# Kernel tuning notes

Hardware: AMD Instinct MI355X
Metric: run time of the kernel (lower is better)

## Reference

```python
import jax, jax.numpy as jnp
import numpy as np

SIGNAL = (32, 32)
KERNEL = (8, 8)
N_FEATURES = [64, 128, 128]
BATCH = 64
ALPHA = 0.5          # source references an undefined global `alpha`; fixed here
LEAKY_SLOPE = 0.01   # torch F.leaky_relu default


def _join_tensor(S, K, loc):
    i = np.arange(S)[:, None, None]
    j = np.arange(S)[None, :, None]
    k = np.arange(K)[None, None, :]
    M = (j >= i) & (i == np.maximum(j, k + loc))
    return jnp.asarray(M.astype(np.float32))


def _meet_tensor(S, K, loc):
    i = np.arange(S)[:, None, None]
    j = np.arange(S)[None, :, None]
    k = np.arange(K)[None, None, :]
    M = (j >= i) & (i == np.minimum(j, k + loc))
    return jnp.asarray(M.astype(np.float32))


def setup_inputs() -> dict:
    key = jax.random.key(0)
    sx, sy = SIGNAL
    kx, ky = KERNEL
    # meet layers use kernel_loc = signal - kernel; join layers use (0, 0)
    cmx = _meet_tensor(sx, kx, sx - kx)
    cmy = _meet_tensor(sy, ky, sy - ky)
    cjx = _join_tensor(sx, kx, 0)
    cjy = _join_tensor(sy, ky, 0)

    keys = jax.random.split(key, 16)
    x = jax.random.normal(keys[0], (BATCH, N_FEATURES[0], sx, sy), dtype=jnp.float32)

    def kaiming(k, shape):
        fan_in = shape[0] * shape[1] * shape[2]  # kx*ky*in_features
        return jax.random.normal(k, shape, dtype=jnp.float32) * np.float32(np.sqrt(2.0 / fan_in))

    inp = {"x": x, "cmx": cmx, "cmy": cmy, "cjx": cjx, "cjy": cjy}
    for li in range(len(N_FEATURES) - 1):
        fi, fo = N_FEATURES[li], N_FEATURES[li + 1]
        inp[f"mw{li}"] = kaiming(keys[1 + 2 * li], (kx, ky, fi, fo))
        inp[f"mb{li}"] = jnp.zeros((fo, 1, 1), dtype=jnp.float32)
        inp[f"jw{li}"] = kaiming(keys[2 + 2 * li], (kx, ky, fi, fo))
        inp[f"jb{li}"] = jnp.zeros((fo, 1, 1), dtype=jnp.float32)
    return inp


def _lattice_conv(cx, cy, X, W, b):
    # Y[m,g,x,y] = sum_{i,j,a,b} cx[i,x,a] cy[j,y,b] X[m,f,i,j] W[a,b,f,g] + bias
    return jnp.einsum('ixa,jyb,mfij,abfg->mgxy', cx, cy, X, W, optimize='optimal') + b


def reference(x, cmx, cmy, cjx, cjy, mw0, mb0, jw0, jb0, mw1, mb1, jw1, jb1):
    params = [(mw0, mb0, jw0, jb0), (mw1, mb1, jw1, jb1)]
    for mw, mb, jw, jb in params:
        m = _lattice_conv(cmx, cmy, x, mw, mb)
        j = _lattice_conv(cjx, cjy, x, jw, jb)
        x = jax.nn.leaky_relu((1.0 - ALPHA) * m + ALPHA * j, negative_slope=LEAKY_SLOPE)
    return x
```

## Files before the change

kernel.cpp:

```cpp
#include <hip/hip_runtime.h>
#include <stdint.h>


typedef __attribute__((ext_vector_type(8))) short short8;
typedef __attribute__((ext_vector_type(4))) float floatx4;

__device__ __forceinline__ float bf2f(unsigned short u) {
  union { uint32_t u; float f; } c; c.u = ((uint32_t)u) << 16; return c.f;
}
__device__ __forceinline__ unsigned short f2bf(float f) {
  union { float f; uint32_t u; } c; c.f = f;
  uint32_t u = c.u;
  uint32_t r = (u + 0x7FFFu + ((u >> 16) & 1u)) >> 16;
  return (unsigned short)r;
}

__global__ void detect_dtype(const unsigned short* __restrict__ xa,
                             int* __restrict__ flag) {
  __shared__ int cnt;
  if (threadIdx.x == 0) cnt = 0;
  __syncthreads();
  unsigned short v = xa[threadIdx.x];
  int e = (v >> 7) & 0xFF;
  int ok = (v == 0) || (e >= 110 && e <= 140);
  atomicAdd(&cnt, ok);
  __syncthreads();
  if (threadIdx.x == 0) *flag = (cnt >= 240) ? 0 : 1;
}

__global__ __launch_bounds__(256) void transpose_in(
    const unsigned short* __restrict__ s16, const float* __restrict__ s32,
    unsigned short* __restrict__ dst, int R, int C,
    const int* __restrict__ flag) {
  __shared__ unsigned short tile[32][33];
  int fp32 = *flag;
  int tx = threadIdx.x, ty = threadIdx.y;
  int c0 = blockIdx.x * 32, r0 = blockIdx.y * 32;
  if (fp32) {
#pragma unroll
    for (int i = 0; i < 32; i += 8)
      tile[ty + i][tx] = f2bf(s32[(size_t)(r0 + ty + i) * C + (c0 + tx)]);
  } else {
#pragma unroll
    for (int i = 0; i < 32; i += 8)
      tile[ty + i][tx] = s16[(size_t)(r0 + ty + i) * C + (c0 + tx)];
  }
  __syncthreads();
#pragma unroll
  for (int i = 0; i < 32; i += 8)
    dst[(size_t)(c0 + ty + i) * R + (r0 + tx)] = tile[tx][ty + i];
}

__global__ __launch_bounds__(256) void transpose_out(
    const unsigned short* __restrict__ src, unsigned short* __restrict__ d16,
    float* __restrict__ d32, int R, int C, const int* __restrict__ flag) {
  __shared__ unsigned short tile[32][33];
  int fp32 = *flag;
  int tx = threadIdx.x, ty = threadIdx.y;
  int c0 = blockIdx.x * 32, r0 = blockIdx.y * 32;
#pragma unroll
  for (int i = 0; i < 32; i += 8)
    tile[ty + i][tx] = src[(size_t)(r0 + ty + i) * C + (c0 + tx)];
  __syncthreads();
  if (fp32) {
#pragma unroll
    for (int i = 0; i < 32; i += 8)
      d32[(size_t)(c0 + ty + i) * R + (r0 + tx)] = bf2f(tile[tx][ty + i]);
  } else {
#pragma unroll
    for (int i = 0; i < 32; i += 8)
      d16[(size_t)(c0 + ty + i) * R + (r0 + tx)] = tile[tx][ty + i];
  }
}

__global__ __launch_bounds__(256) void transpose_w(
    const void* __restrict__ mw, const void* __restrict__ jw,
    float* __restrict__ mwT, float* __restrict__ jwT, int C,
    const int* __restrict__ flag) {
  const void* src = blockIdx.z ? jw : mw;
  float* dst = blockIdx.z ? jwT : mwT;
  __shared__ float tile[32][33];
  int fp32 = *flag;
  int tx = threadIdx.x, ty = threadIdx.y;
  int c0 = blockIdx.x * 32, r0 = blockIdx.y * 32;
#pragma unroll
  for (int i = 0; i < 32; i += 8) {
    size_t idx = (size_t)(r0 + ty + i) * C + (c0 + tx);
    tile[ty + i][tx] = fp32 ? ((const float*)src)[idx]
                            : bf2f(((const unsigned short*)src)[idx]);
  }
  __syncthreads();
#pragma unroll
  for (int i = 0; i < 32; i += 8)
    dst[(size_t)(c0 + ty + i) * 64 + (r0 + tx)] = tile[tx][ty + i];
}

#define SLOT_W1 0
#define SLOT_SB 225
#define SLOT_AS 289
#define SLOT_M  353
#define N_SLOTS 417

template <int F, int G>
__global__ __launch_bounds__(256) void prep_weights2(
    const float* __restrict__ mwT, const float* __restrict__ jwT,
    unsigned short* __restrict__ Wall) {
  int tid = blockIdx.x * 256 + threadIdx.x;
  if (tid >= F * G) return;
  int group = blockIdx.y;
  int f = tid % F, g = tid / F;
  const size_t WS = (size_t)G * F;
  unsigned short* wout = Wall + (size_t)g * F + f;

  float w[64];
  {
    const float4* p = (const float4*)(mwT + (size_t)(f * G + g) * 64);
#pragma unroll
    for (int i = 0; i < 16; ++i) {
      float4 v = p[i];
      w[4 * i] = v.x; w[4 * i + 1] = v.y; w[4 * i + 2] = v.z; w[4 * i + 3] = v.w;
    }
  }
  if (group == 3) {
#pragma unroll
    for (int ab = 0; ab < 64; ++ab)
      wout[(size_t)(SLOT_M + ab) * WS] = f2bf(0.5f * w[ab]);
    return;
  }
#pragma unroll
  for (int a = 0; a < 8; ++a)
#pragma unroll
    for (int b = 6; b >= 0; --b) w[a * 8 + b] += w[a * 8 + b + 1];
  if (group == 2) {
#pragma unroll
    for (int ab = 0; ab < 64; ++ab)
      wout[(size_t)(SLOT_AS + ab) * WS] = f2bf(0.5f * w[ab]);
  }
#pragma unroll
  for (int a = 6; a >= 0; --a)
#pragma unroll
    for (int b = 0; b < 8; ++b) w[a * 8 + b] += w[(a + 1) * 8 + b];
  if (group == 2) {
#pragma unroll
    for (int px = 0; px < 8; ++px)
#pragma unroll
      for (int b = 0; b < 8; ++b) {
        float v = w[px * 8 + b] - (b < 7 ? w[px * 8 + b + 1] : 0.0f);
        wout[(size_t)(SLOT_SB + px * 8 + b) * WS] = f2bf(0.5f * v);
      }
    return;
  }
  float pp[64];
  {
    const float4* p = (const float4*)(jwT + (size_t)(f * G + g) * 64);
#pragma unroll
    for (int i = 0; i < 16; ++i) {
      float4 v = p[i];
      pp[4 * i] = v.x; pp[4 * i + 1] = v.y; pp[4 * i + 2] = v.z; pp[4 * i + 3] = v.w;
    }
  }
#pragma unroll
  for (int a = 0; a < 8; ++a)
#pragma unroll
    for (int b = 1; b < 8; ++b) pp[a * 8 + b] += pp[a * 8 + b - 1];
#pragma unroll
  for (int a = 1; a < 8; ++a)
#pragma unroll
    for (int b = 0; b < 8; ++b) pp[a * 8 + b] += pp[(a - 1) * 8 + b];
  int cx0 = (group == 0) ? 0 : 7, cx1 = (group == 0) ? 7 : 15;
  for (int cx = cx0; cx < cx1; ++cx) {
    int pmx = cx < 7 ? cx : 7;
    int pxx = cx > 7 ? cx - 7 : 0;
#pragma unroll
    for (int cy = 0; cy < 15; ++cy) {
      int pmy = cy < 7 ? cy : 7;
      int pyy = cy > 7 ? cy - 7 : 0;
      float v = 0.5f * (w[pxx * 8 + pyy] + pp[pmx * 8 + pmy]);
      wout[(size_t)(SLOT_W1 + cx * 15 + cy) * WS] = f2bf(v);
    }
  }
}

__global__ void prep_bias2(const void* __restrict__ mb0,
                           const void* __restrict__ jb0,
                           const void* __restrict__ mb1,
                           const void* __restrict__ jb1,
                           float* __restrict__ bias0,
                           float* __restrict__ bias1,
                           const int* __restrict__ flag) {
  int fp32 = *flag;
  int g = threadIdx.x & 127;
  const void* mb = (threadIdx.x < 128) ? mb0 : mb1;
  const void* jb = (threadIdx.x < 128) ? jb0 : jb1;
  float* bo = (threadIdx.x < 128) ? bias0 : bias1;
  float m = fp32 ? ((const float*)mb)[g] : bf2f(((const unsigned short*)mb)[g]);
  float j = fp32 ? ((const float*)jb)[g] : bf2f(((const unsigned short*)jb)[g]);
  bo[g] = 0.5f * (m + j);
}

template <int F>
__device__ __forceinline__ void mfma_tile(
    const unsigned short* __restrict__ A, const unsigned short* __restrict__ W,
    floatx4 acc[8], int wave, int n, int q) {
  const unsigned short* a_ptr = A + ((size_t)(wave * 16 + n)) * F + q * 8;
  const unsigned short* w_ptr = W + (size_t)n * F + q * 8;
#pragma unroll
  for (int kk = 0; kk < F; kk += 32) {
    short8 av = *(const short8*)(a_ptr + kk);
#pragma unroll
    for (int t = 0; t < 8; ++t) {
      short8 bv = *(const short8*)(w_ptr + (size_t)t * 16 * F + kk);
      acc[t] = __builtin_amdgcn_mfma_f32_16x16x32_bf16(av, bv, acc[t], 0, 0, 0);
    }
  }
}

template <int F>
__global__ __launch_bounds__(256) void corr_gemm(
    const unsigned short* __restrict__ Xt, const unsigned short* __restrict__ Wall,
    float* __restrict__ V, float* __restrict__ U, float* __restrict__ T) {
  int bid = blockIdx.x;
  int wave = threadIdx.x >> 6, lane = threadIdx.x & 63;
  int n = lane & 15, q = lane >> 4;
  int ipos, slot;
  float* out;
  if (bid < 256) {
    int a = bid >> 5, y = bid & 31;
    int py = y > 24 ? y - 24 : 0;
    ipos = (24 + a) * 32 + y;
    slot = SLOT_AS + a * 8 + py;
    out = V + (size_t)(a * 32 + y) * 8192;
  } else if (bid < 512) {
    int i = bid - 256;
    int b = i >> 5, x = i & 31;
    int px = x > 24 ? x - 24 : 0;
    ipos = x * 32 + 24 + b;
    slot = SLOT_SB + px * 8 + b;
    out = U + (size_t)(b * 32 + x) * 8192;
  } else {
    int i = bid - 512;
    int a = i >> 3, b = i & 7;
    ipos = (24 + a) * 32 + 24 + b;
    slot = SLOT_M + a * 8 + b;
    out = T + (size_t)(a * 8 + b) * 8192;
  }
  floatx4 acc[8];
#pragma unroll
  for (int t = 0; t < 8; ++t) acc[t] = (floatx4){0.f, 0.f, 0.f, 0.f};
  mfma_tile<F>(Xt + (size_t)ipos * 64 * F, Wall + (size_t)slot * 128 * F,
               acc, wave, n, q);
#pragma unroll
  for (int t = 0; t < 8; ++t) {
    int gcol = t * 16 + n;
#pragma unroll
    for (int r = 0; r < 4; ++r) {
      int m = wave * 16 + q * 4 + r;
      out[(size_t)m * 128 + gcol] = acc[t][r];
    }
  }
}

__global__ __launch_bounds__(256) void scan_corr(float* __restrict__ V,
                                                 float* __restrict__ U,
                                                 float* __restrict__ T) {
  int b = blockIdx.x;
  if (b < 2048) {
    float* base = (b < 1024) ? V : U;
    int tid = ((b & 1023) * 256 + threadIdx.x);
    float* p = base + (size_t)tid;
    float s = 0.f;
#pragma unroll
    for (int a = 0; a < 8; ++a) {
      s += p[(size_t)a * 262144];
      p[(size_t)a * 262144] = s;
    }
  } else {
    int mg = (b - 2048) * 256 + threadIdx.x;
    float col[8];
#pragma unroll
    for (int i = 0; i < 8; ++i) col[i] = 0.f;
#pragma unroll
    for (int a = 0; a < 8; ++a) {
      float rs = 0.f;
#pragma unroll
      for (int bb = 0; bb < 8; ++bb) {
        size_t idx = (size_t)(a * 8 + bb) * 8192 + mg;
        col[bb] += T[idx];
        rs += col[bb];
        T[idx] = rs;
      }
    }
  }
}

template <int F>
__global__ __launch_bounds__(256) void final_gemm(
    const unsigned short* __restrict__ Xt, const unsigned short* __restrict__ Wall,
    const float* __restrict__ V, const float* __restrict__ U,
    const float* __restrict__ T, const float* __restrict__ bias,
    unsigned short* __restrict__ Out) {
  int pos = blockIdx.x;
  int x = pos >> 5, y = pos & 31;
  int wave = threadIdx.x >> 6, lane = threadIdx.x & 63;
  int n = lane & 15, q = lane >> 4;
  int clsx = x < 7 ? x : (x <= 24 ? 7 : x - 17);
  int clsy = y < 7 ? y : (y <= 24 ? 7 : y - 17);
  int px = x > 24 ? x - 24 : 0;
  int py = y > 24 ? y - 24 : 0;
  floatx4 acc[8];
#pragma unroll
  for (int t = 0; t < 8; ++t) acc[t] = (floatx4){0.f, 0.f, 0.f, 0.f};
  mfma_tile<F>(Xt + (size_t)pos * 64 * F,
               Wall + (size_t)(SLOT_W1 + clsx * 15 + clsy) * 128 * F,
               acc, wave, n, q);
  const float* c3 = px ? V + ((size_t)(px - 1) * 32 + y) * 8192 : nullptr;
  const float* c2 = py ? U + ((size_t)(py - 1) * 32 + x) * 8192 : nullptr;
  const float* c4 =
      (px && py) ? T + (size_t)((px - 1) * 8 + (py - 1)) * 8192 : nullptr;
  unsigned short* o = Out + (size_t)pos * 64 * 128;
#pragma unroll
  for (int t = 0; t < 8; ++t) {
    int gcol = t * 16 + n;
    float bv = bias[gcol];
#pragma unroll
    for (int r = 0; r < 4; ++r) {
      int m = wave * 16 + q * 4 + r;
      size_t idx = (size_t)m * 128 + gcol;
      float v = acc[t][r] + bv;
      if (c3) v += c3[idx];
      if (c2) v += c2[idx];
      if (c4) v += c4[idx];
      v = v > 0.f ? v : 0.01f * v;
      o[idx] = f2bf(v);
    }
  }
}

extern "C" void kernel_launch(void* const* d_in, const int* in_sizes, int n_in,
                              void* d_out, int out_size, void* d_ws,
                              size_t ws_size, hipStream_t stream) {
  const void* x   = d_in[0];
  const void* mw0 = d_in[5];
  const void* mb0 = d_in[6];
  const void* jw0 = d_in[7];
  const void* jb0 = d_in[8];
  const void* mw1 = d_in[9];
  const void* mb1 = d_in[10];
  const void* jw1 = d_in[11];
  const void* jb1 = d_in[12];

  char* ws = (char*)d_ws;
  const size_t MB = 1u << 20;
  float*          mwT  = (float*)(ws + 0);
  float*          jwT  = (float*)(ws + 4 * MB + (512u << 10));
  unsigned short* Xt0  = (unsigned short*)(ws + 9 * MB);
  unsigned short* Out2 = (unsigned short*)(ws + 0);
  unsigned short* A1   = (unsigned short*)(ws + 18 * MB);
  unsigned short* WallR = (unsigned short*)(ws + 35 * MB);
  float* bias0 = (float*)(ws + 49 * MB);
  float* bias1 = bias0 + 128;
  int*   flag  = (int*)(bias1 + 128);
  float* V = (float*)d_out;
  float* U = V + (size_t)8 * 32 * 8192;
  float* T = U + (size_t)8 * 32 * 8192;

  detect_dtype<<<1, 256, 0, stream>>>((const unsigned short*)x, flag);

  dim3 tb(32, 8);
  transpose_in<<<dim3(32, 128), tb, 0, stream>>>(
      (const unsigned short*)x, (const float*)x, Xt0, 4096, 1024, flag);
  prep_bias2<<<1, 256, 0, stream>>>(mb0, jb0, mb1, jb1, bias0, bias1, flag);

  transpose_w<<<dim3(8192 / 32, 2, 2), tb, 0, stream>>>(mw0, jw0, mwT, jwT,
                                                        8192, flag);
  prep_weights2<64, 128><<<dim3(32, 4), 256, 0, stream>>>(mwT, jwT, WallR);
  corr_gemm<64><<<576, 256, 0, stream>>>(Xt0, WallR, V, U, T);
  scan_corr<<<2080, 256, 0, stream>>>(V, U, T);
  final_gemm<64><<<1024, 256, 0, stream>>>(Xt0, WallR, V, U, T, bias0, A1);

  transpose_w<<<dim3(16384 / 32, 2, 2), tb, 0, stream>>>(mw1, jw1, mwT, jwT,
                                                         16384, flag);
  prep_weights2<128, 128><<<dim3(64, 4), 256, 0, stream>>>(mwT, jwT, WallR);
  corr_gemm<128><<<576, 256, 0, stream>>>(A1, WallR, V, U, T);
  scan_corr<<<2080, 256, 0, stream>>>(V, U, T);
  final_gemm<128><<<1024, 256, 0, stream>>>(A1, WallR, V, U, T, bias1, Out2);

  transpose_out<<<dim3(256, 32), tb, 0, stream>>>(
      Out2, (unsigned short*)d_out, (float*)d_out, 1024, 8192, flag);
}
```

Measured before the change: 287.6 us.

## Batch weight prep for both layers and split GEMM output columns across blocks

Merges dtype detection with bias prep, and merges the two per-layer weight transpose and prep launches into single launches that cover both layers, with separate workspace buffers. The corr_gemm and final_gemm kernels now split the 128 output channels into two 64-wide halves on a second grid dimension, doubling block count and halving accumulators per block. final_gemm loads the correction terms before the MFMA loop so their latency can overlap with compute. This cuts launch count and raises parallelism, at the cost of reading the A tile twice and a larger workspace footprint.

```diff
diff --git a/kernel.cpp b/kernel.cpp
--- a/kernel.cpp
+++ b/kernel.cpp
@@ -15,8 +15,14 @@
   return (unsigned short)r;
 }
 
-__global__ void detect_dtype(const unsigned short* __restrict__ xa,
-                             int* __restrict__ flag) {
+__global__ void detect_and_bias(const unsigned short* __restrict__ xa,
+                                const void* __restrict__ mb0,
+                                const void* __restrict__ jb0,
+                                const void* __restrict__ mb1,
+                                const void* __restrict__ jb1,
+                                float* __restrict__ bias0,
+                                float* __restrict__ bias1,
+                                int* __restrict__ flag) {
   __shared__ int cnt;
   if (threadIdx.x == 0) cnt = 0;
   __syncthreads();
@@ -25,7 +31,15 @@
   int ok = (v == 0) || (e >= 110 && e <= 140);
   atomicAdd(&cnt, ok);
   __syncthreads();
-  if (threadIdx.x == 0) *flag = (cnt >= 240) ? 0 : 1;
+  int fp32 = (cnt >= 240) ? 0 : 1;
+  if (threadIdx.x == 0) *flag = fp32;
+  int g = threadIdx.x & 127;
+  const void* mb = (threadIdx.x < 128) ? mb0 : mb1;
+  const void* jb = (threadIdx.x < 128) ? jb0 : jb1;
+  float* bo = (threadIdx.x < 128) ? bias0 : bias1;
+  float m = fp32 ? ((const float*)mb)[g] : bf2f(((const unsigned short*)mb)[g]);
+  float j = fp32 ? ((const float*)jb)[g] : bf2f(((const unsigned short*)jb)[g]);
+  bo[g] = 0.5f * (m + j);
 }
 
 __global__ __launch_bounds__(256) void transpose_in(
@@ -73,16 +87,22 @@
   }
 }
 
-__global__ __launch_bounds__(256) void transpose_w(
-    const void* __restrict__ mw, const void* __restrict__ jw,
-    float* __restrict__ mwT, float* __restrict__ jwT, int C,
+__global__ __launch_bounds__(256) void transpose_w4(
+    const void* __restrict__ mw0, const void* __restrict__ jw0,
+    const void* __restrict__ mw1, const void* __restrict__ jw1,
+    float* __restrict__ mwT0, float* __restrict__ jwT0,
+    float* __restrict__ mwT1, float* __restrict__ jwT1,
     const int* __restrict__ flag) {
-  const void* src = blockIdx.z ? jw : mw;
-  float* dst = blockIdx.z ? jwT : mwT;
+  int z = blockIdx.z;
+  const void* src = (z == 0) ? mw0 : (z == 1) ? jw0 : (z == 2) ? mw1 : jw1;
+  float* dst = (z == 0) ? mwT0 : (z == 1) ? jwT0 : (z == 2) ? mwT1 : jwT1;
+  int C = (z < 2) ? 8192 : 16384;
+  int c0 = blockIdx.x * 32;
+  if (c0 >= C) return;
   __shared__ float tile[32][33];
   int fp32 = *flag;
   int tx = threadIdx.x, ty = threadIdx.y;
-  int c0 = blockIdx.x * 32, r0 = blockIdx.y * 32;
+  int r0 = blockIdx.y * 32;
 #pragma unroll
   for (int i = 0; i < 32; i += 8) {
     size_t idx = (size_t)(r0 + ty + i) * C + (c0 + tx);
@@ -101,20 +121,26 @@
 #define SLOT_M  353
 #define N_SLOTS 417
 
-template <int F, int G>
-__global__ __launch_bounds__(256) void prep_weights2(
-    const float* __restrict__ mwT, const float* __restrict__ jwT,
-    unsigned short* __restrict__ Wall) {
+__global__ __launch_bounds__(256) void prep_weights3(
+    const float* __restrict__ mwT0, const float* __restrict__ jwT0,
+    const float* __restrict__ mwT1, const float* __restrict__ jwT1,
+    unsigned short* __restrict__ Wall0, unsigned short* __restrict__ Wall1) {
+  int layer = blockIdx.z;
+  int F = layer ? 128 : 64;
+  int shift = layer ? 7 : 6;
+  const float* mwT = layer ? mwT1 : mwT0;
+  const float* jwT = layer ? jwT1 : jwT0;
+  unsigned short* Wall = layer ? Wall1 : Wall0;
   int tid = blockIdx.x * 256 + threadIdx.x;
-  if (tid >= F * G) return;
+  if (tid >= (F << 7)) return;
   int group = blockIdx.y;
-  int f = tid % F, g = tid / F;
-  const size_t WS = (size_t)G * F;
+  int f = tid & (F - 1), g = tid >> shift;
+  const size_t WS = (size_t)128 * F;
   unsigned short* wout = Wall + (size_t)g * F + f;
 
   float w[64];
   {
-    const float4* p = (const float4*)(mwT + (size_t)(f * G + g) * 64);
+    const float4* p = (const float4*)(mwT + ((size_t)f * 128 + g) * 64);
 #pragma unroll
     for (int i = 0; i < 16; ++i) {
       float4 v = p[i];
@@ -152,7 +178,7 @@
   }
   float pp[64];
   {
-    const float4* p = (const float4*)(jwT + (size_t)(f * G + g) * 64);
+    const float4* p = (const float4*)(jwT + ((size_t)f * 128 + g) * 64);
 #pragma unroll
     for (int i = 0; i < 16; ++i) {
       float4 v = p[i];
@@ -181,34 +207,17 @@
   }
 }
 
-__global__ void prep_bias2(const void* __restrict__ mb0,
-                           const void* __restrict__ jb0,
-                           const void* __restrict__ mb1,
-                           const void* __restrict__ jb1,
-                           float* __restrict__ bias0,
-                           float* __restrict__ bias1,
-                           const int* __restrict__ flag) {
-  int fp32 = *flag;
-  int g = threadIdx.x & 127;
-  const void* mb = (threadIdx.x < 128) ? mb0 : mb1;
-  const void* jb = (threadIdx.x < 128) ? jb0 : jb1;
-  float* bo = (threadIdx.x < 128) ? bias0 : bias1;
-  float m = fp32 ? ((const float*)mb)[g] : bf2f(((const unsigned short*)mb)[g]);
-  float j = fp32 ? ((const float*)jb)[g] : bf2f(((const unsigned short*)jb)[g]);
-  bo[g] = 0.5f * (m + j);
-}
-
-template <int F>
+template <int F, int NT>
 __device__ __forceinline__ void mfma_tile(
     const unsigned short* __restrict__ A, const unsigned short* __restrict__ W,
-    floatx4 acc[8], int wave, int n, int q) {
+    floatx4 acc[NT], int wave, int n, int q) {
   const unsigned short* a_ptr = A + ((size_t)(wave * 16 + n)) * F + q * 8;
   const unsigned short* w_ptr = W + (size_t)n * F + q * 8;
 #pragma unroll
   for (int kk = 0; kk < F; kk += 32) {
     short8 av = *(const short8*)(a_ptr + kk);
 #pragma unroll
-    for (int t = 0; t < 8; ++t) {
+    for (int t = 0; t < NT; ++t) {
       short8 bv = *(const short8*)(w_ptr + (size_t)t * 16 * F + kk);
       acc[t] = __builtin_amdgcn_mfma_f32_16x16x32_bf16(av, bv, acc[t], 0, 0, 0);
     }
@@ -219,7 +228,7 @@
 __global__ __launch_bounds__(256) void corr_gemm(
     const unsigned short* __restrict__ Xt, const unsigned short* __restrict__ Wall,
     float* __restrict__ V, float* __restrict__ U, float* __restrict__ T) {
-  int bid = blockIdx.x;
+  int bid = blockIdx.x, gs = blockIdx.y;
   int wave = threadIdx.x >> 6, lane = threadIdx.x & 63;
   int n = lane & 15, q = lane >> 4;
   int ipos, slot;
@@ -244,14 +253,14 @@
     slot = SLOT_M + a * 8 + b;
     out = T + (size_t)(a * 8 + b) * 8192;
   }
-  floatx4 acc[8];
-#pragma unroll
-  for (int t = 0; t < 8; ++t) acc[t] = (floatx4){0.f, 0.f, 0.f, 0.f};
-  mfma_tile<F>(Xt + (size_t)ipos * 64 * F, Wall + (size_t)slot * 128 * F,
-               acc, wave, n, q);
-#pragma unroll
-  for (int t = 0; t < 8; ++t) {
-    int gcol = t * 16 + n;
+  floatx4 acc[4];
+#pragma unroll
+  for (int t = 0; t < 4; ++t) acc[t] = (floatx4){0.f, 0.f, 0.f, 0.f};
+  mfma_tile<F, 4>(Xt + (size_t)ipos * 64 * F,
+                  Wall + ((size_t)slot * 128 + gs * 64) * F, acc, wave, n, q);
+#pragma unroll
+  for (int t = 0; t < 4; ++t) {
+    int gcol = gs * 64 + t * 16 + n;
 #pragma unroll
     for (int r = 0; r < 4; ++r) {
       int m = wave * 16 + q * 4 + r;
@@ -299,7 +308,7 @@
     const float* __restrict__ V, const float* __restrict__ U,
     const float* __restrict__ T, const float* __restrict__ bias,
     unsigned short* __restrict__ Out) {
-  int pos = blockIdx.x;
+  int pos = blockIdx.x, gs = blockIdx.y;
   int x = pos >> 5, y = pos & 31;
   int wave = threadIdx.x >> 6, lane = threadIdx.x & 63;
   int n = lane & 15, q = lane >> 4;
@@ -307,31 +316,45 @@
   int clsy = y < 7 ? y : (y <= 24 ? 7 : y - 17);
   int px = x > 24 ? x - 24 : 0;
   int py = y > 24 ? y - 24 : 0;
-  floatx4 acc[8];
-#pragma unroll
-  for (int t = 0; t < 8; ++t) acc[t] = (floatx4){0.f, 0.f, 0.f, 0.f};
-  mfma_tile<F>(Xt + (size_t)pos * 64 * F,
-               Wall + (size_t)(SLOT_W1 + clsx * 15 + clsy) * 128 * F,
-               acc, wave, n, q);
   const float* c3 = px ? V + ((size_t)(px - 1) * 32 + y) * 8192 : nullptr;
   const float* c2 = py ? U + ((size_t)(py - 1) * 32 + x) * 8192 : nullptr;
   const float* c4 =
       (px && py) ? T + (size_t)((px - 1) * 8 + (py - 1)) * 8192 : nullptr;
-  unsigned short* o = Out + (size_t)pos * 64 * 128;
-#pragma unroll
-  for (int t = 0; t < 8; ++t) {
-    int gcol = t * 16 + n;
+
+  float csum[4][4];
+#pragma unroll
+  for (int t = 0; t < 4; ++t) {
+    int gcol = gs * 64 + t * 16 + n;
     float bv = bias[gcol];
 #pragma unroll
     for (int r = 0; r < 4; ++r) {
       int m = wave * 16 + q * 4 + r;
       size_t idx = (size_t)m * 128 + gcol;
-      float v = acc[t][r] + bv;
+      float v = bv;
       if (c3) v += c3[idx];
       if (c2) v += c2[idx];
       if (c4) v += c4[idx];
+      csum[t][r] = v;
+    }
+  }
+
+  floatx4 acc[4];
+#pragma unroll
+  for (int t = 0; t < 4; ++t) acc[t] = (floatx4){0.f, 0.f, 0.f, 0.f};
+  mfma_tile<F, 4>(Xt + (size_t)pos * 64 * F,
+                  Wall + ((size_t)(SLOT_W1 + clsx * 15 + clsy) * 128 + gs * 64) * F,
+                  acc, wave, n, q);
+
+  unsigned short* o = Out + (size_t)pos * 64 * 128;
+#pragma unroll
+  for (int t = 0; t < 4; ++t) {
+    int gcol = gs * 64 + t * 16 + n;
+#pragma unroll
+    for (int r = 0; r < 4; ++r) {
+      int m = wave * 16 + q * 4 + r;
+      float v = acc[t][r] + csum[t][r];
       v = v > 0.f ? v : 0.01f * v;
-      o[idx] = f2bf(v);
+      o[(size_t)m * 128 + gcol] = f2bf(v);
     }
   }
 }
@@ -351,39 +374,40 @@
 
   char* ws = (char*)d_ws;
   const size_t MB = 1u << 20;
-  float*          mwT  = (float*)(ws + 0);
-  float*          jwT  = (float*)(ws + 4 * MB + (512u << 10));
-  unsigned short* Xt0  = (unsigned short*)(ws + 9 * MB);
-  unsigned short* Out2 = (unsigned short*)(ws + 0);
-  unsigned short* A1   = (unsigned short*)(ws + 18 * MB);
-  unsigned short* WallR = (unsigned short*)(ws + 35 * MB);
-  float* bias0 = (float*)(ws + 49 * MB);
+  unsigned short* Xt0   = (unsigned short*)(ws + 0);
+  unsigned short* A1    = (unsigned short*)(ws + 9 * MB);
+  unsigned short* Wall0 = (unsigned short*)(ws + 26 * MB);
+  unsigned short* Wall1 = (unsigned short*)(ws + 33 * MB);
+  float* mwT0 = (float*)(ws + 47 * MB);
+  float* jwT0 = (float*)(ws + 50 * MB);
+  float* mwT1 = (float*)(ws + 53 * MB);
+  float* jwT1 = (float*)(ws + 58 * MB);
+  unsigned short* Out2 = (unsigned short*)(ws + 63 * MB);
+  float* bias0 = (float*)(ws + 80 * MB);
   float* bias1 = bias0 + 128;
   int*   flag  = (int*)(bias1 + 128);
   float* V = (float*)d_out;
   float* U = V + (size_t)8 * 32 * 8192;
   float* T = U + (size_t)8 * 32 * 8192;
 
-  detect_dtype<<<1, 256, 0, stream>>>((const unsigned short*)x, flag);
-
   dim3 tb(32, 8);
+  detect_and_bias<<<1, 256, 0, stream>>>((const unsigned short*)x, mb0, jb0,
+                                         mb1, jb1, bias0, bias1, flag);
+  transpose_w4<<<dim3(512, 2, 4), tb, 0, stream>>>(mw0, jw0, mw1, jw1, mwT0,
+                                                   jwT0, mwT1, jwT1, flag);
+  prep_weights3<<<dim3(64, 4, 2), 256, 0, stream>>>(mwT0, jwT0, mwT1, jwT1,
+                                                    Wall0, Wall1);
   transpose_in<<<dim3(32, 128), tb, 0, stream>>>(
       (const unsigned short*)x, (const float*)x, Xt0, 4096, 1024, flag);
-  prep_bias2<<<1, 256, 0, stream>>>(mb0, jb0, mb1, jb1, bias0, bias1, flag);
-
-  transpose_w<<<dim3(8192 / 32, 2, 2), tb, 0, stream>>>(mw0, jw0, mwT, jwT,
-                                                        8192, flag);
-  prep_weights2<64, 128><<<dim3(32, 4), 256, 0, stream>>>(mwT, jwT, WallR);
-  corr_gemm<64><<<576, 256, 0, stream>>>(Xt0, WallR, V, U, T);
+
+  corr_gemm<64><<<dim3(576, 2), 256, 0, stream>>>(Xt0, Wall0, V, U, T);
   scan_corr<<<2080, 256, 0, stream>>>(V, U, T);
-  final_gemm<64><<<1024, 256, 0, stream>>>(Xt0, WallR, V, U, T, bias0, A1);
-
-  transpose_w<<<dim3(16384 / 32, 2, 2), tb, 0, stream>>>(mw1, jw1, mwT, jwT,
-                                                         16384, flag);
-  prep_weights2<128, 128><<<dim3(64, 4), 256, 0, stream>>>(mwT, jwT, WallR);
-  corr_gemm<128><<<576, 256, 0, stream>>>(A1, WallR, V, U, T);
+  final_gemm<64><<<dim3(1024, 2), 256, 0, stream>>>(Xt0, Wall0, V, U, T,
+                                                    bias0, A1);
+  corr_gemm<128><<<dim3(576, 2), 256, 0, stream>>>(A1, Wall1, V, U, T);
   scan_corr<<<2080, 256, 0, stream>>>(V, U, T);
-  final_gemm<128><<<1024, 256, 0, stream>>>(A1, WallR, V, U, T, bias1, Out2);
+  final_gemm<128><<<dim3(1024, 2), 256, 0, stream>>>(A1, Wall1, V, U, T,
+                                                     bias1, Out2);
 
   transpose_out<<<dim3(256, 32), tb, 0, stream>>>(
       Out2, (unsigned short*)d_out, (float*)d_out, 1024, 8192, flag);
```

Result: faster. 264.2 us (-8.1%).
